# Kernel optimization log

Hardware: AMD Instinct MI355X
Metric: run time of the kernel (lower is better)

The kernel has to match this reference:

```python
import jax, jax.numpy as jnp
import numpy as np

B, N, D = 2, 2048, 2048
H, HKV, HD = 16, 4, 128  # n_heads, n_kv_heads, head_dim
G = H // HKV             # GQA group size


def setup_inputs() -> dict:
    key = jax.random.key(0)
    ks = jax.random.split(key, 5)
    x = jax.random.normal(ks[0], (B, N, D), jnp.float32)
    # rotary angles: standard 10000-base frequencies, half head_dim
    inv_freq = 1.0 / (10000.0 ** (jnp.arange(HD // 2, dtype=jnp.float32) / (HD // 2)))
    ang = jnp.arange(N, dtype=jnp.float32)[:, None] * inv_freq[None, :]  # [N, HD/2]
    cos = jnp.cos(ang)[None, :, None, :]  # [1, N, 1, HD/2]
    sin = jnp.sin(ang)[None, :, None, :]
    attn_mask = jnp.ones((B, N), jnp.float32)
    s = 0.02
    Wq = jax.random.normal(ks[1], (D, H * HD), jnp.float32) * s
    Wkv = jax.random.normal(ks[2], (D, 2 * HKV * HD), jnp.float32) * s
    Wo = jax.random.normal(ks[3], (H * HD, D), jnp.float32) * s
    bo = jnp.zeros((D,), jnp.float32)
    return {"x": x, "cos": cos, "sin": sin, "attn_mask": attn_mask,
            "Wq": Wq, "Wkv": Wkv, "Wo": Wo, "bo": bo}


def _rope(t, cos, sin):
    # t: [b, n, h, d]; rotate-half style split at d//2
    d2 = t.shape[-1] // 2
    t1, t2 = t[..., :d2], t[..., d2:]
    return jnp.concatenate([t1 * cos + t2 * sin, t2 * cos - t1 * sin], axis=-1)


def reference(x, cos, sin, attn_mask, Wq, Wkv, Wo, bo):
    b, n, _ = x.shape
    q = (x @ Wq).reshape(b, n, H, HD)
    kv = x @ Wkv
    k, v = jnp.split(kv, 2, axis=-1)
    k = k.reshape(b, n, HKV, HD)
    v = v.reshape(b, n, HKV, HD)
    q = _rope(q, cos, sin)
    k = _rope(k, cos, sin)
    # b n h d -> b h n d; group q heads: head H_idx maps to kv head H_idx % HKV
    # (einops '(r h)' repeat pattern => q reshaped as [b, G, HKV, n, d])
    q = q.transpose(0, 2, 1, 3).reshape(b, G, HKV, n, HD)
    k = k.transpose(0, 2, 1, 3)  # [b, HKV, n, d]
    v = v.transpose(0, 2, 1, 3)
    scale = HD ** -0.5
    attn = jnp.einsum('bghnd,bhmd->bghnm', q, k) * scale
    bias = (1.0 - attn_mask) * -1e9  # [b, n_keys]
    attn = attn + bias[:, None, None, None, :]
    attn = jax.nn.softmax(attn, axis=-1)
    out = jnp.einsum('bghnm,bhmd->bghnd', attn, v)
    # b (g h) n d -> b n (g h d)
    out = out.transpose(0, 3, 1, 2, 4).reshape(b, n, H * HD)
    return out @ Wo + bo
```

## Files before the change

kernel.cpp:

```cpp
#include <hip/hip_runtime.h>
#include <hip/hip_bf16.h>
#include <cstddef>

#define NB    2
#define NSEQ  2048
#define DMODEL 2048
#define NH    16
#define NKV   4
#define HDIM  128

typedef __attribute__((ext_vector_type(8))) short short8;
typedef __attribute__((ext_vector_type(4))) short short4v;
typedef __attribute__((ext_vector_type(4))) float floatx4;
typedef const __attribute__((address_space(1))) void* gptr_t;
typedef __attribute__((address_space(3))) void* lptr_t;

#if __has_builtin(__builtin_amdgcn_exp2f)
#define EXP2F(x) __builtin_amdgcn_exp2f(x)
#else
#define EXP2F(x) __expf((x) * 0.6931471805599453f)
#endif

__device__ inline unsigned short f2bf(float f) {
    unsigned int u = __float_as_uint(f);
    u += 0x7fffu + ((u >> 16) & 1u);
    return (unsigned short)(u >> 16);
}

__device__ inline unsigned int pk2bf_trunc(float a, float b) {
    return __builtin_amdgcn_perm(__float_as_uint(b), __float_as_uint(a), 0x07060302u);
}

__device__ inline floatx4 fzero4() {
    floatx4 v; v[0] = 0.f; v[1] = 0.f; v[2] = 0.f; v[3] = 0.f; return v;
}

__global__ void prep_k(const float* __restrict__ x, const float* __restrict__ Wq,
                       const float* __restrict__ Wkv, const float* __restrict__ Wo,
                       const float* __restrict__ mask,
                       unsigned short* __restrict__ xb,
                       unsigned short* __restrict__ W1T,
                       unsigned short* __restrict__ WoT,
                       float* __restrict__ bias2) {
    __shared__ float tile[32][33];
    const int bid = blockIdx.x, t = threadIdx.x;
    if (bid < 8192) {
        int i = bid * 256 + t;
        float4 v = ((const float4*)x)[i];
        ushort4 o;
        o.x = f2bf(v.x); o.y = f2bf(v.y); o.z = f2bf(v.z); o.w = f2bf(v.w);
        ((ushort4*)xb)[i] = o;
        return;
    }
    if (bid >= 18432) {
        int i = (bid - 18432) * 1024 + t * 4;
        float4 m = *(const float4*)(mask + i);
        const float c = -1.4426950408889634e9f;
        float4 o;
        o.x = (1.f - m.x) * c; o.y = (1.f - m.y) * c;
        o.z = (1.f - m.z) * c; o.w = (1.f - m.w) * c;
        *(float4*)(bias2 + i) = o;
        return;
    }
    const float* W; unsigned short* Wt; int N, local;
    if (bid < 12288)      { W = Wq;  Wt = W1T;                       N = 2048; local = bid - 8192; }
    else if (bid < 14336) { W = Wkv; Wt = W1T + (size_t)2048 * 2048; N = 1024; local = bid - 12288; }
    else                  { W = Wo;  Wt = WoT;                       N = 2048; local = bid - 14336; }
    const int K = 2048;
    int nt = N >> 5;
    int bx = local % nt, by = local / nt;
    int n0 = bx * 32, k0 = by * 32, tx = t & 31, ty = t >> 5;
#pragma unroll
    for (int i = 0; i < 4; i++)
        tile[ty + i * 8][tx] = W[(size_t)(k0 + ty + i * 8) * N + n0 + tx];
    __syncthreads();
#pragma unroll
    for (int i = 0; i < 4; i++)
        Wt[(size_t)(n0 + ty + i * 8) * K + k0 + tx] = f2bf(tile[tx][ty + i * 8]);
}

__global__ __launch_bounds__(256, 3) void gemm_bt(
    const unsigned short* __restrict__ A,
    const unsigned short* __restrict__ Bt,
    float* __restrict__ C,
    const float* __restrict__ bias,
    int M, int N, int K) {
    __shared__ __align__(16) unsigned short As[128 * 32];
    __shared__ __align__(16) unsigned short Bs[128 * 32];
    const int t = threadIdx.x;
    const int chunk = gridDim.x >> 3;
    const int wgid = (blockIdx.x & 7) * chunk + (blockIdx.x >> 3);
    const int nx = N >> 7;
    const int m0 = (wgid / nx) * 128, n0 = (wgid % nx) * 128;
    const int lane = t & 63, wave = t >> 6;
    const int ln = lane & 15, quad = lane >> 4;
    const int wm = (wave >> 1) * 64, wn = (wave & 1) * 64;
    floatx4 acc[4][4];
#pragma unroll
    for (int r = 0; r < 4; r++)
#pragma unroll
        for (int c = 0; c < 4; c++) acc[r][c] = fzero4();

    const int r0 = t >> 2, c0 = (t & 3) * 8;
    const int r1 = (t + 256) >> 2, c1 = ((t + 256) & 3) * 8;

    for (int kt = 0; kt < K; kt += 32) {
        const unsigned short* ga0 = A + (size_t)(m0 + r0) * K + kt + c0;
        const unsigned short* ga1 = A + (size_t)(m0 + r1) * K + kt + c1;
        const unsigned short* gb0 = Bt + (size_t)(n0 + r0) * K + kt + c0;
        const unsigned short* gb1 = Bt + (size_t)(n0 + r1) * K + kt + c1;
        __builtin_amdgcn_global_load_lds((gptr_t)ga0, (lptr_t)(As + t * 8), 16, 0, 0);
        __builtin_amdgcn_global_load_lds((gptr_t)ga1, (lptr_t)(As + (t + 256) * 8), 16, 0, 0);
        __builtin_amdgcn_global_load_lds((gptr_t)gb0, (lptr_t)(Bs + t * 8), 16, 0, 0);
        __builtin_amdgcn_global_load_lds((gptr_t)gb1, (lptr_t)(Bs + (t + 256) * 8), 16, 0, 0);
        __syncthreads();
        short8 af[4], bfr[4];
#pragma unroll
        for (int r = 0; r < 4; r++)
            af[r] = *(const short8*)(As + (wm + r * 16 + ln) * 32 + quad * 8);
#pragma unroll
        for (int c = 0; c < 4; c++)
            bfr[c] = *(const short8*)(Bs + (wn + c * 16 + ln) * 32 + quad * 8);
#pragma unroll
        for (int r = 0; r < 4; r++)
#pragma unroll
            for (int c = 0; c < 4; c++)
                acc[r][c] = __builtin_amdgcn_mfma_f32_16x16x32_bf16(af[r], bfr[c], acc[r][c], 0, 0, 0);
        __syncthreads();
    }
#pragma unroll
    for (int r = 0; r < 4; r++) {
        int mb = m0 + wm + r * 16 + quad * 4;
#pragma unroll
        for (int c = 0; c < 4; c++) {
            int col = n0 + wn + c * 16 + ln;
            float bv = bias ? bias[col] : 0.f;
#pragma unroll
            for (int g = 0; g < 4; g++)
                C[(size_t)(mb + g) * N + col] = acc[r][c][g] + bv;
        }
    }
}

__global__ __launch_bounds__(256, 3) void gemm_qkv_rope(
    const unsigned short* __restrict__ A,
    const unsigned short* __restrict__ Bt,
    const float* __restrict__ cosb,
    const float* __restrict__ sinb,
    unsigned short* __restrict__ Qb,
    unsigned short* __restrict__ Kb,
    unsigned short* __restrict__ Vt) {
    const int K = DMODEL;
    __shared__ __align__(16) unsigned short As[128 * 32];
    __shared__ __align__(16) unsigned short Bs[128 * 32];
    __shared__ __align__(16) unsigned short Vx[128 * 136];
    const int t = threadIdx.x;
    const int wgid = (blockIdx.x & 7) * 96 + (blockIdx.x >> 3);
    const int m0 = (wgid / 24) * 128, n0 = (wgid % 24) * 128;
    const int lane = t & 63, wave = t >> 6;
    const int ln = lane & 15, quad = lane >> 4;
    const int wm = (wave >> 1) * 64, bq = (wave & 1) * 32;
    floatx4 acc[4][4];
#pragma unroll
    for (int r = 0; r < 4; r++)
#pragma unroll
        for (int c = 0; c < 4; c++) acc[r][c] = fzero4();

    const int r0 = t >> 2, c0 = (t & 3) * 8;
    const int r1 = (t + 256) >> 2, c1 = ((t + 256) & 3) * 8;

    for (int kt = 0; kt < K; kt += 32) {
        const unsigned short* ga0 = A + (size_t)(m0 + r0) * K + kt + c0;
        const unsigned short* ga1 = A + (size_t)(m0 + r1) * K + kt + c1;
        const unsigned short* gb0 = Bt + (size_t)(n0 + r0) * K + kt + c0;
        const unsigned short* gb1 = Bt + (size_t)(n0 + r1) * K + kt + c1;
        __builtin_amdgcn_global_load_lds((gptr_t)ga0, (lptr_t)(As + t * 8), 16, 0, 0);
        __builtin_amdgcn_global_load_lds((gptr_t)ga1, (lptr_t)(As + (t + 256) * 8), 16, 0, 0);
        __builtin_amdgcn_global_load_lds((gptr_t)gb0, (lptr_t)(Bs + t * 8), 16, 0, 0);
        __builtin_amdgcn_global_load_lds((gptr_t)gb1, (lptr_t)(Bs + (t + 256) * 8), 16, 0, 0);
        __syncthreads();
        short8 af[4], bfr[4];
#pragma unroll
        for (int r = 0; r < 4; r++)
            af[r] = *(const short8*)(As + (wm + r * 16 + ln) * 32 + quad * 8);
#pragma unroll
        for (int c = 0; c < 4; c++)
            bfr[c] = *(const short8*)(
                Bs + (bq + (c & 1) * 16 + (c >> 1) * 64 + ln) * 32 + quad * 8);
#pragma unroll
        for (int r = 0; r < 4; r++)
#pragma unroll
            for (int c = 0; c < 4; c++)
                acc[r][c] = __builtin_amdgcn_mfma_f32_16x16x32_bf16(af[r], bfr[c], acc[r][c], 0, 0, 0);
        __syncthreads();
    }

    if (n0 < 2048) {
        const float qs = (float)(0.08838834764831845 * 1.4426950408889634);
        int h = n0 >> 7;
#pragma unroll
        for (int r = 0; r < 4; r++)
#pragma unroll
            for (int c = 0; c < 2; c++)
#pragma unroll
                for (int g = 0; g < 4; g++) {
                    int row = m0 + wm + r * 16 + quad * 4 + g;
                    int b = row >> 11, n = row & 2047;
                    int j = bq + c * 16 + ln;
                    float cv = cosb[n * 64 + j], sv = sinb[n * 64 + j];
                    float t1 = acc[r][c][g], t2 = acc[r][c + 2][g];
                    unsigned short* qp = Qb + ((size_t)(b * NH + h) * NSEQ + n) * 128;
                    qp[j]      = f2bf((t1 * cv + t2 * sv) * qs);
                    qp[j + 64] = f2bf((t2 * cv - t1 * sv) * qs);
                }
    } else if (n0 < 2560) {
        int hk = (n0 - 2048) >> 7;
#pragma unroll
        for (int r = 0; r < 4; r++)
#pragma unroll
            for (int c = 0; c < 2; c++)
#pragma unroll
                for (int g = 0; g < 4; g++) {
                    int row = m0 + wm + r * 16 + quad * 4 + g;
                    int b = row >> 11, n = row & 2047;
                    int j = bq + c * 16 + ln;
                    float cv = cosb[n * 64 + j], sv = sinb[n * 64 + j];
                    float t1 = acc[r][c][g], t2 = acc[r][c + 2][g];
                    unsigned short* kp = Kb + ((size_t)(b * NKV + hk) * NSEQ + n) * 128;
                    kp[j]      = f2bf(t1 * cv + t2 * sv);
                    kp[j + 64] = f2bf(t2 * cv - t1 * sv);
                }
    } else {
        int hk = (n0 - 2560) >> 7;
#pragma unroll
        for (int r = 0; r < 4; r++)
#pragma unroll
            for (int c = 0; c < 4; c++) {
                int d = bq + (c & 1) * 16 + (c >> 1) * 64 + ln;
                int s = wm + (r >> 1) * 32 + quad * 8 + (r & 1) * 4;
#pragma unroll
                for (int g = 0; g < 4; g++)
                    Vx[d * 136 + s + g] = f2bf(acc[r][c][g]);
            }
        __syncthreads();
        int b = m0 >> 11, nloc = m0 & 2047;
#pragma unroll
        for (int pass = 0; pass < 2; pass++) {
            int d = pass * 64 + (t >> 2), q4 = t & 3;
            unsigned short* vp =
                Vt + ((size_t)(b * NKV + hk) * 128 + d) * NSEQ + nloc + q4 * 32;
#pragma unroll
            for (int i = 0; i < 4; i++)
                *(short8*)(vp + i * 8) = *(const short8*)(Vx + d * 136 + q4 * 32 + i * 8);
        }
    }
}

__global__ __launch_bounds__(128, 2) void attn_k(
    const unsigned short* __restrict__ Qb,
    const unsigned short* __restrict__ Kb,
    const unsigned short* __restrict__ Vt,
    const float* __restrict__ bias2,
    unsigned short* __restrict__ Ab) {
    __shared__ __align__(16) unsigned short Ks[2 * 32 * 128];
    __shared__ __align__(16) unsigned short Vs[2 * 128 * 32];
    const int t = threadIdx.x, wave = t >> 6, lane = t & 63;
    const int ln = lane & 15, quad = lane >> 4;
    const int id = blockIdx.x;
    const int pair = id & 7, b = pair >> 2, kv = pair & 3;
    const int rest = id >> 3, g4 = rest & 3, h = g4 * 4 + kv, qb = rest >> 2;
    const int q0 = qb * 64;

    const unsigned short* Kbase = Kb + (size_t)(b * NKV + kv) * NSEQ * 128;
    const unsigned short* Vbase = Vt + (size_t)(b * NKV + kv) * 128 * NSEQ;
    const float* bbase = bias2 + b * NSEQ;

    const unsigned short* Qp =
        Qb + ((size_t)(b * NH + h) * NSEQ + q0 + wave * 32 + ln) * 128;
    short8 qf[2][4];
#pragma unroll
    for (int rt = 0; rt < 2; rt++)
#pragma unroll
        for (int kc = 0; kc < 4; kc++)
            qf[rt][kc] = *(const short8*)(Qp + rt * 16 * 128 + kc * 32 + quad * 8);

    const char* kp[4];
#pragma unroll
    for (int kc = 0; kc < 4; kc++)
        kp[kc] = (const char*)Ks + ln * 256 + (((kc * 4 + quad) ^ (ln & 7)) * 16);
    const char* vpp = (const char*)Vs + ln * 64 + ((quad ^ ((ln ^ (ln >> 2)) & 3)) * 16);

    floatx4 Oacc[2][8];
#pragma unroll
    for (int rt = 0; rt < 2; rt++)
#pragma unroll
        for (int d = 0; d < 8; d++) Oacc[rt][d] = fzero4();
    floatx4 Lacc[2];
    Lacc[0] = fzero4(); Lacc[1] = fzero4();

    short8 ones8;
#pragma unroll
    for (int i = 0; i < 8; i++) ones8[i] = (short)0x3F80;

    auto stage = [&](int ktn, int buf) {
#pragma unroll
        for (int i = 0; i < 4; i++) {
            int c = i * 128 + t, r = c >> 4, c8 = c & 15;
            __builtin_amdgcn_global_load_lds(
                (gptr_t)(Kbase + (size_t)(ktn + r) * 128 + ((c8 ^ (r & 7)) * 8)),
                (lptr_t)(Ks + buf * 4096 + c * 8), 16, 0, 0);
        }
#pragma unroll
        for (int i = 0; i < 4; i++) {
            int c = i * 128 + t, dr = c >> 2, c8 = c & 3;
            int f = (dr ^ (dr >> 2)) & 3;
            __builtin_amdgcn_global_load_lds(
                (gptr_t)(Vbase + (size_t)dr * NSEQ + ktn + ((c8 ^ f) * 8)),
                (lptr_t)(Vs + buf * 4096 + c * 8), 16, 0, 0);
        }
    };

    stage(0, 0);
    __syncthreads();

#pragma unroll 1
    for (int it2 = 0; it2 < NSEQ / 64; ++it2) {
#pragma unroll
        for (int half = 0; half < 2; ++half) {
            const int kt = (it2 * 2 + half) * 32;
            const int ktn = (kt + 32) & (NSEQ - 1);
            stage(ktn, half ^ 1);
            const int off = half * 8192;

            floatx4 sacc[2][2];
#pragma unroll
            for (int nj = 0; nj < 2; nj++) {
                floatx4 bv = *(const floatx4*)(bbase + kt + nj * 16 + quad * 4);
                sacc[0][nj] = bv;
                sacc[1][nj] = bv;
            }
            __builtin_amdgcn_s_setprio(1);
#pragma unroll
            for (int kc = 0; kc < 4; kc++) {
                short8 kfv[2];
#pragma unroll
                for (int nj = 0; nj < 2; nj++)
                    kfv[nj] = *(const short8*)(kp[kc] + off + nj * 4096);
#pragma unroll
                for (int rt = 0; rt < 2; rt++)
#pragma unroll
                    for (int nj = 0; nj < 2; nj++)
                        sacc[rt][nj] = __builtin_amdgcn_mfma_f32_16x16x32_bf16(
                            kfv[nj], qf[rt][kc], sacc[rt][nj], 0, 0, 0);
            }
            __builtin_amdgcn_s_setprio(0);

            short8 pf[2];
#pragma unroll
            for (int rt = 0; rt < 2; rt++) {
                union { short8 s; unsigned int w[4]; } pu;
#pragma unroll
                for (int e = 0; e < 2; e++) {
                    float e0 = EXP2F(sacc[rt][e][0]);
                    float e1 = EXP2F(sacc[rt][e][1]);
                    float e2 = EXP2F(sacc[rt][e][2]);
                    float e3 = EXP2F(sacc[rt][e][3]);
                    pu.w[e * 2 + 0] = pk2bf_trunc(e0, e1);
                    pu.w[e * 2 + 1] = pk2bf_trunc(e2, e3);
                }
                pf[rt] = pu.s;
            }

            __builtin_amdgcn_s_setprio(1);
#pragma unroll
            for (int rt = 0; rt < 2; rt++)
                Lacc[rt] = __builtin_amdgcn_mfma_f32_16x16x32_bf16(
                    ones8, pf[rt], Lacc[rt], 0, 0, 0);
#pragma unroll
            for (int dt = 0; dt < 8; dt++) {
                short8 vf = *(const short8*)(vpp + off + dt * 1024);
#pragma unroll
                for (int rt = 0; rt < 2; rt++)
                    Oacc[rt][dt] = __builtin_amdgcn_mfma_f32_16x16x32_bf16(
                        vf, pf[rt], Oacc[rt][dt], 0, 0, 0);
            }
            __builtin_amdgcn_s_setprio(0);
            __syncthreads();
        }
    }

#pragma unroll
    for (int rt = 0; rt < 2; rt++) {
        float inv = 1.f / Lacc[rt][0];
        int row = q0 + wave * 32 + rt * 16 + ln;
        unsigned short* outp = Ab + (size_t)(b * NSEQ + row) * 2048 + h * 128;
#pragma unroll
        for (int dt = 0; dt < 8; dt++) {
            short4v o4;
#pragma unroll
            for (int g = 0; g < 4; g++) o4[g] = (short)f2bf(Oacc[rt][dt][g] * inv);
            *(short4v*)(outp + dt * 16 + quad * 4) = o4;
        }
    }
}

extern "C" void kernel_launch(void* const* d_in, const int* in_sizes, int n_in,
                              void* d_out, int out_size, void* d_ws, size_t ws_size,
                              hipStream_t stream) {
    const float* x    = (const float*)d_in[0];
    const float* cosb = (const float*)d_in[1];
    const float* sinb = (const float*)d_in[2];
    const float* mask = (const float*)d_in[3];
    const float* Wq   = (const float*)d_in[4];
    const float* Wkv  = (const float*)d_in[5];
    const float* Wo   = (const float*)d_in[6];
    const float* bo   = (const float*)d_in[7];
    float* out = (float*)d_out;

    char* ws = (char*)d_ws;
    unsigned short* xb  = (unsigned short*)ws; ws += (size_t)4096 * 2048 * 2;
    unsigned short* W1T = (unsigned short*)ws; ws += (size_t)3072 * 2048 * 2;
    unsigned short* WoT = (unsigned short*)ws; ws += (size_t)2048 * 2048 * 2;
    unsigned short* Qb  = (unsigned short*)ws; ws += (size_t)2 * 16 * 2048 * 128 * 2;
    unsigned short* Kb  = (unsigned short*)ws; ws += (size_t)2 * 4 * 2048 * 128 * 2;
    unsigned short* Vt  = (unsigned short*)ws; ws += (size_t)2 * 4 * 2048 * 128 * 2;
    unsigned short* Ab  = (unsigned short*)ws; ws += (size_t)2 * 2048 * 2048 * 2;
    float* bias2 = (float*)ws;                 ws += (size_t)NB * NSEQ * 4;

    prep_k<<<18436, 256, 0, stream>>>(x, Wq, Wkv, Wo, mask, xb, W1T, WoT, bias2);
    gemm_qkv_rope<<<768, 256, 0, stream>>>(xb, W1T, cosb, sinb, Qb, Kb, Vt);
    attn_k<<<1024, 128, 0, stream>>>(Qb, Kb, Vt, bias2, Ab);
    gemm_bt<<<512, 256, 0, stream>>>(Ab, WoT, out, bo, 4096, 2048, 2048);
}
```

Before: 309.5 us.

## Double-buffer LDS tiles in projection GEMMs and alias V staging buffer

Both the generic GEMM and the fused QKV+RoPE GEMM now keep two LDS buffers for the A and B tiles. The next k-slice is issued with global_load_lds before the current slice is read and run through MFMA, so global latency can overlap compute and the barrier right after the load is gone. In the QKV kernel the V-transpose staging area now shares LDS with the operand buffers, which keeps LDS use from growing and may help occupancy. The cost is one redundant prefetch at the loop end, and correctness relies on the trailing barrier ordering the async LDS writes.

```diff
diff --git a/kernel.cpp b/kernel.cpp
--- a/kernel.cpp
+++ b/kernel.cpp
@@ -85,8 +85,8 @@
     float* __restrict__ C,
     const float* __restrict__ bias,
     int M, int N, int K) {
-    __shared__ __align__(16) unsigned short As[128 * 32];
-    __shared__ __align__(16) unsigned short Bs[128 * 32];
+    __shared__ __align__(16) unsigned short As[2 * 128 * 32];
+    __shared__ __align__(16) unsigned short Bs[2 * 128 * 32];
     const int t = threadIdx.x;
     const int chunk = gridDim.x >> 3;
     const int wgid = (blockIdx.x & 7) * chunk + (blockIdx.x >> 3);
@@ -104,23 +104,36 @@
     const int r0 = t >> 2, c0 = (t & 3) * 8;
     const int r1 = (t + 256) >> 2, c1 = ((t + 256) & 3) * 8;
 
-    for (int kt = 0; kt < K; kt += 32) {
-        const unsigned short* ga0 = A + (size_t)(m0 + r0) * K + kt + c0;
-        const unsigned short* ga1 = A + (size_t)(m0 + r1) * K + kt + c1;
-        const unsigned short* gb0 = Bt + (size_t)(n0 + r0) * K + kt + c0;
-        const unsigned short* gb1 = Bt + (size_t)(n0 + r1) * K + kt + c1;
-        __builtin_amdgcn_global_load_lds((gptr_t)ga0, (lptr_t)(As + t * 8), 16, 0, 0);
-        __builtin_amdgcn_global_load_lds((gptr_t)ga1, (lptr_t)(As + (t + 256) * 8), 16, 0, 0);
-        __builtin_amdgcn_global_load_lds((gptr_t)gb0, (lptr_t)(Bs + t * 8), 16, 0, 0);
-        __builtin_amdgcn_global_load_lds((gptr_t)gb1, (lptr_t)(Bs + (t + 256) * 8), 16, 0, 0);
-        __syncthreads();
+    auto stage = [&](int kt, int buf) {
+        __builtin_amdgcn_global_load_lds(
+            (gptr_t)(A + (size_t)(m0 + r0) * K + kt + c0),
+            (lptr_t)(As + buf * 4096 + t * 8), 16, 0, 0);
+        __builtin_amdgcn_global_load_lds(
+            (gptr_t)(A + (size_t)(m0 + r1) * K + kt + c1),
+            (lptr_t)(As + buf * 4096 + (t + 256) * 8), 16, 0, 0);
+        __builtin_amdgcn_global_load_lds(
+            (gptr_t)(Bt + (size_t)(n0 + r0) * K + kt + c0),
+            (lptr_t)(Bs + buf * 4096 + t * 8), 16, 0, 0);
+        __builtin_amdgcn_global_load_lds(
+            (gptr_t)(Bt + (size_t)(n0 + r1) * K + kt + c1),
+            (lptr_t)(Bs + buf * 4096 + (t + 256) * 8), 16, 0, 0);
+    };
+
+    stage(0, 0);
+    __syncthreads();
+
+#pragma unroll 1
+    for (int it = 0; it < K / 32; ++it) {
+        const int buf = it & 1;
+        const int ktn = ((it + 1) * 32) & (K - 1);
+        stage(ktn, buf ^ 1);
         short8 af[4], bfr[4];
 #pragma unroll
         for (int r = 0; r < 4; r++)
-            af[r] = *(const short8*)(As + (wm + r * 16 + ln) * 32 + quad * 8);
+            af[r] = *(const short8*)(As + buf * 4096 + (wm + r * 16 + ln) * 32 + quad * 8);
 #pragma unroll
         for (int c = 0; c < 4; c++)
-            bfr[c] = *(const short8*)(Bs + (wn + c * 16 + ln) * 32 + quad * 8);
+            bfr[c] = *(const short8*)(Bs + buf * 4096 + (wn + c * 16 + ln) * 32 + quad * 8);
 #pragma unroll
         for (int r = 0; r < 4; r++)
 #pragma unroll
@@ -151,9 +164,10 @@
     unsigned short* __restrict__ Kb,
     unsigned short* __restrict__ Vt) {
     const int K = DMODEL;
-    __shared__ __align__(16) unsigned short As[128 * 32];
-    __shared__ __align__(16) unsigned short Bs[128 * 32];
-    __shared__ __align__(16) unsigned short Vx[128 * 136];
+    __shared__ __align__(16) unsigned char smem[128 * 136 * 2];
+    unsigned short* As = (unsigned short*)smem;
+    unsigned short* Bs = (unsigned short*)(smem + 16384);
+    unsigned short* Vx = (unsigned short*)smem;
     const int t = threadIdx.x;
     const int wgid = (blockIdx.x & 7) * 96 + (blockIdx.x >> 3);
     const int m0 = (wgid / 24) * 128, n0 = (wgid % 24) * 128;
@@ -169,24 +183,37 @@
     const int r0 = t >> 2, c0 = (t & 3) * 8;
     const int r1 = (t + 256) >> 2, c1 = ((t + 256) & 3) * 8;
 
-    for (int kt = 0; kt < K; kt += 32) {
-        const unsigned short* ga0 = A + (size_t)(m0 + r0) * K + kt + c0;
-        const unsigned short* ga1 = A + (size_t)(m0 + r1) * K + kt + c1;
-        const unsigned short* gb0 = Bt + (size_t)(n0 + r0) * K + kt + c0;
-        const unsigned short* gb1 = Bt + (size_t)(n0 + r1) * K + kt + c1;
-        __builtin_amdgcn_global_load_lds((gptr_t)ga0, (lptr_t)(As + t * 8), 16, 0, 0);
-        __builtin_amdgcn_global_load_lds((gptr_t)ga1, (lptr_t)(As + (t + 256) * 8), 16, 0, 0);
-        __builtin_amdgcn_global_load_lds((gptr_t)gb0, (lptr_t)(Bs + t * 8), 16, 0, 0);
-        __builtin_amdgcn_global_load_lds((gptr_t)gb1, (lptr_t)(Bs + (t + 256) * 8), 16, 0, 0);
-        __syncthreads();
+    auto stage = [&](int kt, int buf) {
+        __builtin_amdgcn_global_load_lds(
+            (gptr_t)(A + (size_t)(m0 + r0) * K + kt + c0),
+            (lptr_t)(As + buf * 4096 + t * 8), 16, 0, 0);
+        __builtin_amdgcn_global_load_lds(
+            (gptr_t)(A + (size_t)(m0 + r1) * K + kt + c1),
+            (lptr_t)(As + buf * 4096 + (t + 256) * 8), 16, 0, 0);
+        __builtin_amdgcn_global_load_lds(
+            (gptr_t)(Bt + (size_t)(n0 + r0) * K + kt + c0),
+            (lptr_t)(Bs + buf * 4096 + t * 8), 16, 0, 0);
+        __builtin_amdgcn_global_load_lds(
+            (gptr_t)(Bt + (size_t)(n0 + r1) * K + kt + c1),
+            (lptr_t)(Bs + buf * 4096 + (t + 256) * 8), 16, 0, 0);
+    };
+
+    stage(0, 0);
+    __syncthreads();
+
+#pragma unroll 1
+    for (int it = 0; it < K / 32; ++it) {
+        const int buf = it & 1;
+        const int ktn = ((it + 1) * 32) & (K - 1);
+        stage(ktn, buf ^ 1);
         short8 af[4], bfr[4];
 #pragma unroll
         for (int r = 0; r < 4; r++)
-            af[r] = *(const short8*)(As + (wm + r * 16 + ln) * 32 + quad * 8);
+            af[r] = *(const short8*)(As + buf * 4096 + (wm + r * 16 + ln) * 32 + quad * 8);
 #pragma unroll
         for (int c = 0; c < 4; c++)
             bfr[c] = *(const short8*)(
-                Bs + (bq + (c & 1) * 16 + (c >> 1) * 64 + ln) * 32 + quad * 8);
+                Bs + buf * 4096 + (bq + (c & 1) * 16 + (c >> 1) * 64 + ln) * 32 + quad * 8);
 #pragma unroll
         for (int r = 0; r < 4; r++)
 #pragma unroll
```

After: 304.1 us, median of 2. Within noise of the previous version (-1.7%).
